# Optimization experiments

Measured on AMD Instinct MI355X. Metric: run time of the kernel, lower is better.

Reference implementation:

```python
import jax, jax.numpy as jnp
import numpy as np

B, S, DM = 2, 4096, 512
H, D = 8, 64          # heads, size_per_head
BS = 64               # block size (from == to)
NB = S // BS          # 64 blocks
R = 3                 # num random blocks per middle row


def setup_inputs() -> dict:
    key = jax.random.key(0)
    ks = jax.random.split(key, 8)
    sc = 0.02
    x = jax.random.normal(ks[0], (B, S, DM), dtype=jnp.float32)
    w_q = jax.random.normal(ks[1], (DM, H * D), dtype=jnp.float32) * sc
    b_q = jnp.zeros((H * D,), dtype=jnp.float32)
    w_k = jax.random.normal(ks[2], (DM, H * D), dtype=jnp.float32) * sc
    b_k = jnp.zeros((H * D,), dtype=jnp.float32)
    w_v = jax.random.normal(ks[3], (DM, H * D), dtype=jnp.float32) * sc
    b_v = jnp.zeros((H * D,), dtype=jnp.float32)
    # random attention adjacency: per head, rows 1..NB-2, r random middle blocks
    rand_attn = jax.random.randint(ks[4], (H, NB - 2, R), 1, NB - 1, dtype=jnp.int32)
    return {"x": x, "w_q": w_q, "b_q": b_q, "w_k": w_k, "b_k": b_k,
            "w_v": w_v, "b_v": b_v, "rand_attn": rand_attn}


def _bigbird_attention(q, k, v, rand_attn):
    # q,k,v: [B,H,S,D]; rand_attn: [H,NB-2,R]
    scale = 1.0 / jnp.sqrt(jnp.asarray(D, q.dtype))
    qb = q.reshape(B, H, NB, BS, D)
    kb = k.reshape(B, H, NB, BS, D)
    vb = v.reshape(B, H, NB, BS, D)

    # gather random key/value blocks per head/row: [B,H,NB-2,R*BS,D]
    h_idx = jnp.arange(H)[:, None, None]
    gk = kb[:, h_idx, rand_attn].reshape(B, H, NB - 2, R * BS, D)
    gv = vb[:, h_idx, rand_attn].reshape(B, H, NB - 2, R * BS, D)

    # --- row 0: global, full attention ---
    s0 = jnp.einsum('bhqd,bhkd->bhqk', qb[:, :, 0], k) * scale
    c0 = jnp.einsum('bhqk,bhkd->bhqd', jax.nn.softmax(s0, axis=-1), v)

    # --- row 1: blocks [0,1,2,last] + rand ---
    k1 = jnp.concatenate([kb[:, :, 0], kb[:, :, 1], kb[:, :, 2],
                          kb[:, :, -1], gk[:, :, 0]], axis=2)
    v1 = jnp.concatenate([vb[:, :, 0], vb[:, :, 1], vb[:, :, 2],
                          vb[:, :, -1], gv[:, :, 0]], axis=2)
    s1 = jnp.einsum('bhqd,bhkd->bhqk', qb[:, :, 1], k1) * scale
    c1 = jnp.einsum('bhqk,bhkd->bhqd', jax.nn.softmax(s1, axis=-1), v1)

    # --- middle rows i = 2 .. NB-3: first + band(i-1,i,i+1) + rand + last ---
    q_mid = qb[:, :, 2:NB - 2]                                  # [B,H,M,BS,D]
    band_k = jnp.concatenate([kb[:, :, 1:NB - 3], kb[:, :, 2:NB - 2],
                              kb[:, :, 3:NB - 1]], axis=3)       # [B,H,M,3BS,D]
    band_v = jnp.concatenate([vb[:, :, 1:NB - 3], vb[:, :, 2:NB - 2],
                              vb[:, :, 3:NB - 1]], axis=3)
    gk_mid = gk[:, :, 1:NB - 3]                                  # [B,H,M,R*BS,D]
    gv_mid = gv[:, :, 1:NB - 3]
    s_first = jnp.einsum('bhmqd,bhkd->bhmqk', q_mid, kb[:, :, 0])
    s_band = jnp.einsum('bhmqd,bhmkd->bhmqk', q_mid, band_k)
    s_rand = jnp.einsum('bhmqd,bhmkd->bhmqk', q_mid, gk_mid)
    s_last = jnp.einsum('bhmqd,bhkd->bhmqk', q_mid, kb[:, :, -1])
    s_mid = jnp.concatenate([s_first, s_band, s_rand, s_last], axis=-1) * scale
    p = jax.nn.softmax(s_mid, axis=-1)
    p_first = p[..., :BS]
    p_band = p[..., BS:4 * BS]
    p_rand = p[..., 4 * BS:4 * BS + R * BS]
    p_last = p[..., 4 * BS + R * BS:]
    c_mid = (jnp.einsum('bhmqk,bhkd->bhmqd', p_first, vb[:, :, 0])
             + jnp.einsum('bhmqk,bhmkd->bhmqd', p_band, band_v)
             + jnp.einsum('bhmqk,bhmkd->bhmqd', p_rand, gv_mid)
             + jnp.einsum('bhmqk,bhkd->bhmqd', p_last, vb[:, :, -1]))

    # --- row NB-2: blocks [0, NB-3, NB-2, last] + rand ---
    k2 = jnp.concatenate([kb[:, :, 0], kb[:, :, -3], kb[:, :, -2],
                          kb[:, :, -1], gk[:, :, -1]], axis=2)
    v2 = jnp.concatenate([vb[:, :, 0], vb[:, :, -3], vb[:, :, -2],
                          vb[:, :, -1], gv[:, :, -1]], axis=2)
    s2 = jnp.einsum('bhqd,bhkd->bhqk', qb[:, :, -2], k2) * scale
    c2 = jnp.einsum('bhqk,bhkd->bhqd', jax.nn.softmax(s2, axis=-1), v2)

    # --- last row: global, full attention ---
    s3 = jnp.einsum('bhqd,bhkd->bhqk', qb[:, :, -1], k) * scale
    c3 = jnp.einsum('bhqk,bhkd->bhqd', jax.nn.softmax(s3, axis=-1), v)

    ctx = jnp.concatenate([c0[:, :, None], c1[:, :, None], c_mid,
                           c2[:, :, None], c3[:, :, None]], axis=2)
    return ctx.reshape(B, H, S, D)


def reference(x, w_q, b_q, w_k, b_k, w_v, b_v, rand_attn):
    q = (x @ w_q + b_q).reshape(B, S, H, D).transpose(0, 2, 1, 3)
    k = (x @ w_k + b_k).reshape(B, S, H, D).transpose(0, 2, 1, 3)
    v = (x @ w_v + b_v).reshape(B, S, H, D).transpose(0, 2, 1, 3)
    ctx = _bigbird_attention(q, k, v, rand_attn)  # [B,H,S,D]
    return ctx.transpose(0, 2, 1, 3).reshape(B, S, H * D)
```

## Files before the change

kernel.cpp:

```cpp
#include <hip/hip_runtime.h>
#include <stdint.h>

#define BB 2
#define SS 4096
#define DM 512
#define HH 8
#define DD 64
#define NB 64
#define RR 3

typedef __attribute__((ext_vector_type(8))) short short8;
typedef __attribute__((ext_vector_type(4))) float f4;

__device__ __forceinline__ unsigned short f2bf(float f) {
    unsigned u = __float_as_uint(f);
    unsigned r = (u + 0x7fffu + ((u >> 16) & 1u)) >> 16;
    return (unsigned short)r;
}

__device__ __forceinline__ void g2l16(const void* g, void* l) {
    __builtin_amdgcn_global_load_lds(
        (const __attribute__((address_space(1))) unsigned int*)g,
        (__attribute__((address_space(3))) unsigned int*)l, 16, 0, 0);
}

__global__ __launch_bounds__(256) void cvt_kernel(
    const float* __restrict__ x,
    const float* __restrict__ wq,
    const float* __restrict__ wk,
    const float* __restrict__ wv,
    unsigned short* __restrict__ xb,
    unsigned short* __restrict__ wbT)
{
    __shared__ unsigned short Ts[64][68];
    const int t = threadIdx.x;
    const int bid = blockIdx.x;
    if (bid < 2048) {
        int i0 = bid * 512 + t;
#pragma unroll
        for (int p = 0; p < 2; ++p) {
            float4 v = reinterpret_cast<const float4*>(x)[i0 + p * 256];
            ushort4 o;
            o.x = f2bf(v.x); o.y = f2bf(v.y); o.z = f2bf(v.z); o.w = f2bf(v.w);
            reinterpret_cast<ushort4*>(xb)[i0 + p * 256] = o;
        }
    } else {
        int bid2 = bid - 2048;
        int which = bid2 >> 6;
        int tile = bid2 & 63;
        int tr = tile >> 3, tc = tile & 7;
        const float* w = (which == 0) ? wq : (which == 1) ? wk : wv;
        int r = t >> 2, c0 = (t & 3) * 16;
        const float* src = w + (size_t)(tr * 64 + r) * 512 + tc * 64 + c0;
#pragma unroll
        for (int j = 0; j < 4; ++j) {
            float4 v = *reinterpret_cast<const float4*>(src + j * 4);
            Ts[r][c0 + j * 4 + 0] = f2bf(v.x);
            Ts[r][c0 + j * 4 + 1] = f2bf(v.y);
            Ts[r][c0 + j * 4 + 2] = f2bf(v.z);
            Ts[r][c0 + j * 4 + 3] = f2bf(v.w);
        }
        __syncthreads();
        unsigned short* dst = wbT + (size_t)(which * 512 + tc * 64 + r) * 512 + tr * 64 + c0;
        short8 o0, o1;
#pragma unroll
        for (int j = 0; j < 8; ++j) {
            ((unsigned short*)&o0)[j] = Ts[c0 + j][r];
            ((unsigned short*)&o1)[j] = Ts[c0 + 8 + j][r];
        }
        *reinterpret_cast<short8*>(dst) = o0;
        *reinterpret_cast<short8*>(dst + 8) = o1;
    }
}

__global__ __launch_bounds__(256) void qkv_gemm(
    const unsigned short* __restrict__ xb,
    const unsigned short* __restrict__ wbT,
    const float* __restrict__ bq,
    const float* __restrict__ bk,
    const float* __restrict__ bv,
    unsigned short* __restrict__ qb,
    unsigned short* __restrict__ kb,
    unsigned short* __restrict__ vT)
{
    __shared__ __attribute__((aligned(16))) unsigned short As[64 * 64];
    __shared__ __attribute__((aligned(16))) unsigned short Bs[128 * 64];
    const int tid = threadIdx.x;
    const int l = tid & 63;
    const int w = tid >> 6;
    const int wr = w >> 1, wc = w & 1;
    const int lq = l & 15, lg = l >> 4;
    const int bid = blockIdx.x;
    const int rb = (bid & 7) * 192 + (bid >> 3);
    const int tn = rb % 12, tm = rb / 12;

    const int srow = l >> 3;
    const int sg = (l & 7) ^ srow;
    const unsigned short* ag = xb + (size_t)(tm * 64 + w * 16 + srow) * DM + sg * 8;
    const unsigned short* bg = wbT + (size_t)(tn * 128 + w * 32 + srow) * DM + sg * 8;
    char* al = reinterpret_cast<char*>(As) + w * 2048;
    char* bl = reinterpret_cast<char*>(Bs) + w * 4096;

    f4 acc[2][4];
#pragma unroll
    for (int m = 0; m < 2; m++)
#pragma unroll
        for (int n = 0; n < 4; n++) acc[m][n] = (f4){0.f, 0.f, 0.f, 0.f};

    for (int kt = 0; kt < 8; ++kt) {
        g2l16(ag + kt * 64, al);
        g2l16(ag + (size_t)8 * DM + kt * 64, al + 1024);
#pragma unroll
        for (int j = 0; j < 4; ++j)
            g2l16(bg + (size_t)j * 8 * DM + kt * 64, bl + j * 1024);
        __syncthreads();
#pragma unroll
        for (int c = 0; c < 2; c++) {
            short8 af[2], bf[4];
#pragma unroll
            for (int m = 0; m < 2; m++) {
                int row = wr * 32 + m * 16 + lq;
                int gs = (c * 4 + lg) ^ (row & 7);
                af[m] = *reinterpret_cast<const short8*>(
                    reinterpret_cast<const char*>(As) + row * 128 + gs * 16);
            }
#pragma unroll
            for (int n = 0; n < 4; n++) {
                int row = wc * 64 + n * 16 + lq;
                int gs = (c * 4 + lg) ^ (row & 7);
                bf[n] = *reinterpret_cast<const short8*>(
                    reinterpret_cast<const char*>(Bs) + row * 128 + gs * 16);
            }
#pragma unroll
            for (int m = 0; m < 2; m++)
#pragma unroll
                for (int n = 0; n < 4; n++)
                    acc[m][n] = __builtin_amdgcn_mfma_f32_16x16x32_bf16(af[m], bf[n], acc[m][n], 0, 0, 0);
        }
        __syncthreads();
    }

#pragma unroll
    for (int m = 0; m < 2; m++) {
        int gm = tm * 64 + wr * 32 + m * 16 + lg * 4;
#pragma unroll
        for (int n = 0; n < 4; n++) {
            int gn = tn * 128 + wc * 64 + n * 16 + lq;
            int which = gn >> 9, hd = gn & 511;
            float bias = ((which == 0) ? bq : (which == 1) ? bk : bv)[hd];
            int h = hd >> 6, d = hd & 63;
#pragma unroll
            for (int r = 0; r < 4; r++) {
                int gmr = gm + r;
                int b = gmr >> 12, s = gmr & 4095;
                unsigned short val = f2bf(acc[m][n][r] + bias);
                if (which == 0)
                    qb[(((size_t)b * HH + h) * SS + s) * DD + d] = val;
                else if (which == 1)
                    kb[(((size_t)b * HH + h) * SS + s) * DD + d] = val;
                else
                    vT[(((size_t)b * HH + h) * DD + d) * SS + s] = val;
            }
        }
    }
}

__global__ __launch_bounds__(256) void bigbird_attn(
    const unsigned short* __restrict__ qb,
    const unsigned short* __restrict__ kb,
    const unsigned short* __restrict__ vT,
    const int* __restrict__ rand_attn,
    float* __restrict__ out,
    float* __restrict__ PO,
    float* __restrict__ PL)
{
    __shared__ __attribute__((aligned(16))) unsigned short Kb[2][4096];
    __shared__ __attribute__((aligned(16))) unsigned short Vb[2][4096];
    __shared__ __attribute__((aligned(16))) unsigned short Pl[4][1024];
    const int tid = threadIdx.x;
    const int l = tid & 63, w = tid >> 6;
    const int lq = l & 15, lg = l >> 4;
    const int bid0 = blockIdx.x;
    const int bid = (bid0 & 7) * 156 + (bid0 >> 3);

    int b, h, qi, e = 0, c = 0;
    int kbl[8];
    float bias7 = 0.f;
    bool partial;
    if (bid < 992) {
        partial = false;
        qi = 1 + bid % 62;
        int t = bid / 62;
        h = t & 7;
        b = t >> 3;
        kbl[0] = 0;
        if (qi == 1)       { kbl[1] = 1;  kbl[2] = 2;  kbl[3] = 63; }
        else if (qi == 62) { kbl[1] = 61; kbl[2] = 62; kbl[3] = 63; }
        else               { kbl[1] = qi - 1; kbl[2] = qi; kbl[3] = qi + 1; }
        const int* ra = rand_attn + (h * 62 + (qi - 1)) * 3;
        kbl[4] = ra[0]; kbl[5] = ra[1]; kbl[6] = ra[2];
        if (qi == 1 || qi == 62) { kbl[7] = 0; bias7 = -30.f; }
        else kbl[7] = 63;
    } else {
        partial = true;
        int idx = bid - 992;
        c = idx & 7;
        e = (idx >> 3) & 1;
        h = (idx >> 4) & 7;
        b = idx >> 7;
        qi = e ? 63 : 0;
#pragma unroll
        for (int i = 0; i < 8; ++i) kbl[i] = c * 8 + i;
    }

    const size_t bh = (size_t)b * HH + h;
    const unsigned short* qp = qb + bh * SS * DD;
    const char* kpB = reinterpret_cast<const char*>(kb + bh * SS * DD);
    const char* vpB = reinterpret_cast<const char*>(vT + bh * (size_t)DD * SS);

    const int qrow = qi * 64 + w * 16 + lq;
    short8 qf[2];
#pragma unroll
    for (int cc = 0; cc < 2; cc++)
        qf[cc] = *reinterpret_cast<const short8*>(qp + (size_t)qrow * DD + cc * 32 + lg * 8);

    const int srow = l >> 3;
    const int sg = (l & 7) ^ srow;

#define STAGE(bufidx, blk)                                                              \
    {                                                                                   \
        const char* kq = kpB + (size_t)(blk) * 8192;                                    \
        const char* vq = vpB + (size_t)(blk) * 128;                                     \
        char* kl = reinterpret_cast<char*>(Kb[bufidx]) + w * 2048;                      \
        char* vl = reinterpret_cast<char*>(Vb[bufidx]) + w * 2048;                      \
        g2l16(kq + (w * 16 + srow) * 128 + sg * 16, kl);                                \
        g2l16(kq + (w * 16 + 8 + srow) * 128 + sg * 16, kl + 1024);                     \
        g2l16(vq + (size_t)(w * 16 + srow) * 8192 + sg * 16, vl);                       \
        g2l16(vq + (size_t)(w * 16 + 8 + srow) * 8192 + sg * 16, vl + 1024);            \
    }

    STAGE(0, kbl[0]);
    __syncthreads();

    float lacc[4] = {0.f, 0.f, 0.f, 0.f};
    f4 oacc[4];
#pragma unroll
    for (int g = 0; g < 4; g++) oacc[g] = (f4){0.f, 0.f, 0.f, 0.f};

    char* pb = reinterpret_cast<char*>(&Pl[w][0]);
    const float scale = 0.125f;

#pragma unroll
    for (int i = 0; i < 8; ++i) {
        const int cur = i & 1;
        if (i < 7) { STAGE(cur ^ 1, kbl[i + 1]); }
        const float bi = (i == 7) ? bias7 : 0.f;
        const char* Kc = reinterpret_cast<const char*>(Kb[cur]);
        const char* Vc = reinterpret_cast<const char*>(Vb[cur]);

        f4 sacc[4];
#pragma unroll
        for (int g = 0; g < 4; g++) sacc[g] = (f4){0.f, 0.f, 0.f, 0.f};
#pragma unroll
        for (int cc = 0; cc < 2; cc++) {
#pragma unroll
            for (int g = 0; g < 4; g++) {
                int row = g * 16 + lq;
                short8 kf = *reinterpret_cast<const short8*>(
                    Kc + row * 128 + (((cc * 4 + lg) ^ (row & 7)) << 4));
                sacc[g] = __builtin_amdgcn_mfma_f32_16x16x32_bf16(qf[cc], kf, sacc[g], 0, 0, 0);
            }
        }

#pragma unroll
        for (int g = 0; g < 4; g++)
#pragma unroll
            for (int r = 0; r < 4; r++) {
                float pv = __expf(fmaf(sacc[g][r], scale, bi));
                lacc[r] += pv;
                int row = lg * 4 + r;
                int colbyte = (g * 16 + lq) * 2;
                int gr = (colbyte >> 4) ^ (row & 7);
                *reinterpret_cast<unsigned short*>(pb + row * 128 + (gr << 4) + (colbyte & 15)) =
                    f2bf(pv);
            }

        short8 pa[2];
#pragma unroll
        for (int cc = 0; cc < 2; cc++) {
            int row = lq;
            int gr = (cc * 4 + lg) ^ (row & 7);
            pa[cc] = *reinterpret_cast<const short8*>(pb + row * 128 + (gr << 4));
        }

#pragma unroll
        for (int cc = 0; cc < 2; cc++)
#pragma unroll
            for (int g = 0; g < 4; g++) {
                int row = g * 16 + lq;
                short8 vf = *reinterpret_cast<const short8*>(
                    Vc + row * 128 + (((cc * 4 + lg) ^ (row & 7)) << 4));
                oacc[g] = __builtin_amdgcn_mfma_f32_16x16x32_bf16(pa[cc], vf, oacc[g], 0, 0, 0);
            }

        __syncthreads();
    }
#undef STAGE

#pragma unroll
    for (int off = 1; off < 16; off <<= 1)
#pragma unroll
        for (int r = 0; r < 4; r++) lacc[r] += __shfl_xor(lacc[r], off, 64);

    if (!partial) {
#pragma unroll
        for (int r = 0; r < 4; r++) {
            float inv = 1.0f / lacc[r];
            int row = lg * 4 + r;
            int s = qi * 64 + w * 16 + row;
#pragma unroll
            for (int g = 0; g < 4; g++) {
                int d = g * 16 + lq;
                out[((size_t)b * SS + s) * DM + h * DD + d] = oacc[g][r] * inv;
            }
        }
    } else {
        int pr = ((b * 8 + h) * 2 + e);
        float* po = PO + ((size_t)(pr * 8 + c) << 12);
        float* pl = PL + (pr * 8 + c) * 64;
#pragma unroll
        for (int r = 0; r < 4; r++) {
            int row = w * 16 + lg * 4 + r;
#pragma unroll
            for (int g = 0; g < 4; g++)
                po[row * 64 + g * 16 + lq] = oacc[g][r];
            if (lq == 0) pl[row] = lacc[r];
        }
    }
}

__global__ __launch_bounds__(256) void bigbird_combine(
    const float* __restrict__ PO,
    const float* __restrict__ PL,
    float* __restrict__ out)
{
    int pr = blockIdx.x;
    int e = pr & 1, h = (pr >> 1) & 7, b = pr >> 4;
    int t = threadIdx.x;
    int row = t >> 2;
    int d0 = (t & 3) * 16;

    float acc[16];
#pragma unroll
    for (int j = 0; j < 16; j++) acc[j] = 0.f;
    float lsum = 0.f;

#pragma unroll
    for (int c = 0; c < 8; c++) {
        const float* po = PO + ((size_t)(pr * 8 + c) << 12) + row * 64 + d0;
#pragma unroll
        for (int j = 0; j < 4; j++) {
            float4 v = *reinterpret_cast<const float4*>(po + j * 4);
            acc[j * 4 + 0] += v.x; acc[j * 4 + 1] += v.y;
            acc[j * 4 + 2] += v.z; acc[j * 4 + 3] += v.w;
        }
        lsum += PL[(pr * 8 + c) * 64 + row];
    }

    int qi = e ? 63 : 0;
    int s = qi * 64 + row;
    float inv = 1.0f / lsum;
    float* op = out + ((size_t)b * SS + s) * DM + h * DD + d0;
#pragma unroll
    for (int j = 0; j < 4; j++) {
        float4 v;
        v.x = acc[j * 4 + 0] * inv; v.y = acc[j * 4 + 1] * inv;
        v.z = acc[j * 4 + 2] * inv; v.w = acc[j * 4 + 3] * inv;
        *reinterpret_cast<float4*>(op + j * 4) = v;
    }
}

extern "C" void kernel_launch(void* const* d_in, const int* in_sizes, int n_in,
                              void* d_out, int out_size, void* d_ws, size_t ws_size,
                              hipStream_t stream) {
    const float* x  = (const float*)d_in[0];
    const float* wq = (const float*)d_in[1];
    const float* bq = (const float*)d_in[2];
    const float* wk = (const float*)d_in[3];
    const float* bk = (const float*)d_in[4];
    const float* wv = (const float*)d_in[5];
    const float* bv = (const float*)d_in[6];
    const int* rand_attn = (const int*)d_in[7];
    float* out = (float*)d_out;

    char* ws = (char*)d_ws;
    unsigned short* xb  = (unsigned short*)ws;
    unsigned short* wbT = (unsigned short*)(ws + 8388608);
    unsigned short* qbp = (unsigned short*)(ws + 9961472);
    unsigned short* kbp = qbp + (size_t)4194304;
    unsigned short* vTp = kbp + (size_t)4194304;
    float* PO = (float*)(ws + 35127296);
    float* PL = (float*)(ws + 35127296 + 4194304);

    hipLaunchKernelGGL(cvt_kernel, dim3(2240), dim3(256), 0, stream, x, wq, wk, wv, xb, wbT);
    hipLaunchKernelGGL(qkv_gemm, dim3(1536), dim3(256), 0, stream, xb, wbT, bq, bk, bv, qbp, kbp, vTp);
    hipLaunchKernelGGL(bigbird_attn, dim3(1248), dim3(256), 0, stream, qbp, kbp, vTp, rand_attn, out, PO, PL);
    hipLaunchKernelGGL(bigbird_combine, dim3(32), dim3(256), 0, stream, PO, PL, out);
}
```

Baseline: 141.3 us.

## Compute transposed S and redistribute P via lane shuffles instead of LDS

Swaps the MFMA operand order so each lane holds scores for a single query row across key columns, packs exp'd probabilities to bf16 with v_cvt_pk_bf16_f32, and rebuilds the A-operand for the PV matmul through cross-lane shuffles rather than a round trip through a per-wave LDS scratch buffer. The row-sum is now a single per-lane scalar reduced with two xor shuffles and broadcast back to rows at the end. This removes the LDS P buffer and its scalar 16-bit stores and reads, and shrinks shared-memory use. In exchange it adds many ds_bpermute shuffles and selects per block, and depends on the lane mapping being exactly right.

```diff
diff --git a/kernel.cpp b/kernel.cpp
--- a/kernel.cpp
+++ b/kernel.cpp
@@ -176,14 +176,13 @@
 {
     __shared__ __attribute__((aligned(16))) unsigned short Kb[2][4096];
     __shared__ __attribute__((aligned(16))) unsigned short Vb[2][4096];
-    __shared__ __attribute__((aligned(16))) unsigned short Pl[4][1024];
     const int tid = threadIdx.x;
     const int l = tid & 63, w = tid >> 6;
     const int lq = l & 15, lg = l >> 4;
     const int bid0 = blockIdx.x;
     const int bid = (bid0 & 7) * 156 + (bid0 >> 3);
 
-    int b, h, qi, e = 0, c = 0;
+    int b, h, qi, e2 = 0, c = 0;
     int kbl[8];
     float bias7 = 0.f;
     bool partial;
@@ -205,10 +204,10 @@
         partial = true;
         int idx = bid - 992;
         c = idx & 7;
-        e = (idx >> 3) & 1;
+        e2 = (idx >> 3) & 1;
         h = (idx >> 4) & 7;
         b = idx >> 7;
-        qi = e ? 63 : 0;
+        qi = e2 ? 63 : 0;
 #pragma unroll
         for (int i = 0; i < 8; ++i) kbl[i] = c * 8 + i;
     }
@@ -242,13 +241,15 @@
     STAGE(0, kbl[0]);
     __syncthreads();
 
-    float lacc[4] = {0.f, 0.f, 0.f, 0.f};
+    float lacc = 0.f;
     f4 oacc[4];
 #pragma unroll
     for (int g = 0; g < 4; g++) oacc[g] = (f4){0.f, 0.f, 0.f, 0.f};
 
-    char* pb = reinterpret_cast<char*>(&Pl[w][0]);
     const float scale = 0.125f;
+    const int e = (lg & 1) * 2;
+    const int hi = lg >> 1;
+    const int s0 = lq + e * 16, s1 = s0 + 16;
 
 #pragma unroll
     for (int i = 0; i < 8; ++i) {
@@ -268,29 +269,43 @@
                 int row = g * 16 + lq;
                 short8 kf = *reinterpret_cast<const short8*>(
                     Kc + row * 128 + (((cc * 4 + lg) ^ (row & 7)) << 4));
-                sacc[g] = __builtin_amdgcn_mfma_f32_16x16x32_bf16(qf[cc], kf, sacc[g], 0, 0, 0);
-            }
-        }
-
-#pragma unroll
-        for (int g = 0; g < 4; g++)
-#pragma unroll
-            for (int r = 0; r < 4; r++) {
-                float pv = __expf(fmaf(sacc[g][r], scale, bi));
-                lacc[r] += pv;
-                int row = lg * 4 + r;
-                int colbyte = (g * 16 + lq) * 2;
-                int gr = (colbyte >> 4) ^ (row & 7);
-                *reinterpret_cast<unsigned short*>(pb + row * 128 + (gr << 4) + (colbyte & 15)) =
-                    f2bf(pv);
-            }
+                sacc[g] = __builtin_amdgcn_mfma_f32_16x16x32_bf16(kf, qf[cc], sacc[g], 0, 0, 0);
+            }
+        }
+
+        unsigned pkw[8];
+#pragma unroll
+        for (int g = 0; g < 4; g++) {
+            float p0 = __expf(fmaf(sacc[g][0], scale, bi));
+            float p1 = __expf(fmaf(sacc[g][1], scale, bi));
+            float p2 = __expf(fmaf(sacc[g][2], scale, bi));
+            float p3 = __expf(fmaf(sacc[g][3], scale, bi));
+            lacc += (p0 + p1) + (p2 + p3);
+            unsigned r0, r1;
+            asm("v_cvt_pk_bf16_f32 %0, %1, %2" : "=v"(r0) : "v"(p0), "v"(p1));
+            asm("v_cvt_pk_bf16_f32 %0, %1, %2" : "=v"(r1) : "v"(p2), "v"(p3));
+            pkw[g * 2] = r0; pkw[g * 2 + 1] = r1;
+        }
 
         short8 pa[2];
 #pragma unroll
         for (int cc = 0; cc < 2; cc++) {
-            int row = lq;
-            int gr = (cc * 4 + lg) ^ (row & 7);
-            pa[cc] = *reinterpret_cast<const short8*>(pb + row * 128 + (gr << 4));
+            unsigned A0 = pkw[cc * 4 + 0], A1 = pkw[cc * 4 + 1];
+            unsigned B0 = pkw[cc * 4 + 2], B1 = pkw[cc * 4 + 3];
+            unsigned wA0 = (unsigned)__shfl((int)A0, s0, 64);
+            unsigned wA1 = (unsigned)__shfl((int)A1, s0, 64);
+            unsigned wA2 = (unsigned)__shfl((int)A0, s1, 64);
+            unsigned wA3 = (unsigned)__shfl((int)A1, s1, 64);
+            unsigned wB0 = (unsigned)__shfl((int)B0, s0, 64);
+            unsigned wB1 = (unsigned)__shfl((int)B1, s0, 64);
+            unsigned wB2 = (unsigned)__shfl((int)B0, s1, 64);
+            unsigned wB3 = (unsigned)__shfl((int)B1, s1, 64);
+            union { unsigned u[4]; short8 v; } pu;
+            pu.u[0] = hi ? wB0 : wA0;
+            pu.u[1] = hi ? wB1 : wA1;
+            pu.u[2] = hi ? wB2 : wA2;
+            pu.u[3] = hi ? wB3 : wA3;
+            pa[cc] = pu.v;
         }
 
 #pragma unroll
@@ -307,15 +322,16 @@
     }
 #undef STAGE
 
-#pragma unroll
-    for (int off = 1; off < 16; off <<= 1)
-#pragma unroll
-        for (int r = 0; r < 4; r++) lacc[r] += __shfl_xor(lacc[r], off, 64);
+    lacc += __shfl_xor(lacc, 16, 64);
+    lacc += __shfl_xor(lacc, 32, 64);
+    float ls[4];
+#pragma unroll
+    for (int r = 0; r < 4; r++) ls[r] = __shfl(lacc, lg * 4 + r, 64);
 
     if (!partial) {
 #pragma unroll
         for (int r = 0; r < 4; r++) {
-            float inv = 1.0f / lacc[r];
+            float inv = 1.0f / ls[r];
             int row = lg * 4 + r;
             int s = qi * 64 + w * 16 + row;
 #pragma unroll
@@ -325,7 +341,7 @@
             }
         }
     } else {
-        int pr = ((b * 8 + h) * 2 + e);
+        int pr = ((b * 8 + h) * 2 + e2);
         float* po = PO + ((size_t)(pr * 8 + c) << 12);
         float* pl = PL + (pr * 8 + c) * 64;
 #pragma unroll
@@ -334,7 +350,7 @@
 #pragma unroll
             for (int g = 0; g < 4; g++)
                 po[row * 64 + g * 16 + lq] = oacc[g][r];
-            if (lq == 0) pl[row] = lacc[r];
+            if (lq == 0) pl[row] = ls[r];
         }
     }
 }
```

After: 144.6 us. 1.02x slower.
